# Kernel tuning notes

Hardware: AMD Instinct MI355X
Metric: run time of the kernel (lower is better)

Reference implementation:

```python
import jax, jax.numpy as jnp
import numpy as np

N_USERS = 100000
N_ITEMS = 50000
DIM = 64
HID = 64
E = 3200000
B = 16384


def setup_inputs() -> dict:
    key = jax.random.key(0)
    ks = jax.random.split(key, 16)
    N = N_USERS + N_ITEMS
    return {
        "users": jax.random.randint(ks[0], (B,), 0, N_USERS),
        "items": jax.random.randint(ks[1], (B,), 0, N_ITEMS),
        "edge_index": jax.random.randint(ks[2], (2, E), 0, N),
        "edge_weight": jax.random.uniform(ks[3], (E,), dtype=jnp.float32),
        # learned parameters
        "U": jax.random.normal(ks[4], (N_USERS, DIM), jnp.float32) * 0.1,
        "I": jax.random.normal(ks[5], (N_ITEMS, DIM), jnp.float32) * 0.1,
        "W0": jax.random.normal(ks[6], (DIM, HID), jnp.float32) / np.sqrt(DIM),
        "b0": jnp.zeros((HID,), jnp.float32),
        "g0": jnp.ones((HID,), jnp.float32),
        "be0": jnp.zeros((HID,), jnp.float32),
        "W1": jax.random.normal(ks[7], (HID, HID), jnp.float32) / np.sqrt(HID),
        "b1": jnp.zeros((HID,), jnp.float32),
        "g1": jnp.ones((HID,), jnp.float32),
        "be1": jnp.zeros((HID,), jnp.float32),
        "Wp": jax.random.normal(ks[8], (HID, DIM), jnp.float32) / np.sqrt(HID),
        "bp": jnp.zeros((DIM,), jnp.float32),
        "bu": jnp.zeros((N_USERS,), jnp.float32),
        "bi": jnp.zeros((N_ITEMS,), jnp.float32),
        "mu": jnp.zeros((), jnp.float32),
    }


def _layernorm(h, g, b, eps=1e-5):
    m = jnp.mean(h, axis=-1, keepdims=True)
    v = jnp.mean(jnp.square(h - m), axis=-1, keepdims=True)
    return (h - m) * jax.lax.rsqrt(v + eps) * g + b


def reference(users, items, edge_index, edge_weight, U, I,
              W0, b0, g0, be0, W1, b1, g1, be1, Wp, bp, bu, bi, mu):
    N = U.shape[0] + I.shape[0]
    x = jnp.concatenate([U, I], axis=0)  # [N, DIM]

    # GCN normalization with added self-loops (torch_geometric gcn_norm)
    loop = jnp.arange(N)
    src = jnp.concatenate([edge_index[0], loop])
    dst = jnp.concatenate([edge_index[1], loop])
    ew = jnp.concatenate([edge_weight, jnp.ones((N,), edge_weight.dtype)])
    deg = jax.ops.segment_sum(ew, dst, num_segments=N)
    dinv = jnp.where(deg > 0, jax.lax.rsqrt(deg), 0.0)
    norm = dinv[src] * ew * dinv[dst]  # [E+N]

    def conv(h, W, b):
        hw = h @ W  # [N, HID]
        msgs = norm[:, None] * hw[src]  # gather: [E+N, HID]
        return jax.ops.segment_sum(msgs, dst, num_segments=N) + b

    # layer 0: conv -> layernorm -> relu -> (dropout=identity, eval) -> residual
    h = x
    h_in = h
    h = conv(h, W0, b0)
    h = jax.nn.relu(_layernorm(h, g0, be0)) + h_in
    # layer 1
    h_in = h
    h = conv(h, W1, b1)
    h = jax.nn.relu(_layernorm(h, g1, be1)) + h_in

    h = h @ Wp + bp  # proj_out: [N, DIM]
    h_user = h[:U.shape[0]]
    h_item = h[U.shape[0]:]

    s = jnp.sum(h_user[users] * h_item[items], axis=-1)
    s = s + bu[users] + bi[items] + mu
    return jnp.clip(s, 1.0, 5.0)
```

## Files before the change

### kernel.cpp

```cpp
#include <hip/hip_runtime.h>

#define NU 100000
#define NI 50000
#define NN 150000
#define D  64
#define CAP 47
#define OVF_MAX 4096

#define BINSHIFT 9
#define BINW 512
#define NBINS 293
#define BINCAP 11448
#define STAGE_CAP 20
#define EPT 4
#define SPILL_CAP 262144

typedef unsigned int uint;
typedef unsigned short ushort;

__device__ __forceinline__ float wave_reduce_add(float v) {
    #pragma unroll
    for (int m = 32; m >= 1; m >>= 1) v += __shfl_xor(v, m, 64);
    return v;
}
__device__ __forceinline__ float bf2f(ushort u) {
    union { uint i; float f; } c; c.i = ((uint)u) << 16; return c.f;
}
__device__ __forceinline__ ushort f2bf(float f) {
    union { float f; uint i; } c; c.f = f;
    uint r = c.i + 0x7FFF + ((c.i >> 16) & 1);
    return (ushort)(r >> 16);
}
__device__ __forceinline__ float lane_bcast(float v, int l) {
    return __int_as_float(__builtin_amdgcn_readlane(__float_as_int(v), l));
}
__device__ __forceinline__ uint q14(float w) {
    int q = (int)(w * 16384.0f);
    q = (q < 0) ? 0 : (q > 16383 ? 16383 : q);
    return (uint)q;
}
__device__ __forceinline__ void spill_one(int d, uint s, float w,
        uint2* __restrict__ spill, int* __restrict__ spillcnt) {
    int si = atomicAdd(spillcnt, 1);
    if (si < SPILL_CAP) spill[si] = make_uint2(s | (q14(w) << 18), (uint)d);
}

__global__ __launch_bounds__(256) void k_bin(
        const int* __restrict__ src, const int* __restrict__ dst,
        const float* __restrict__ ew, int* __restrict__ bincur,
        uint2* __restrict__ binbuf, uint2* __restrict__ spill,
        int* __restrict__ spillcnt, int E) {
    __shared__ uint2 stage[NBINS][STAGE_CAP];
    __shared__ int scnt[NBINS];
    int t = threadIdx.x;
    for (int i = t; i < NBINS; i += 256) scnt[i] = 0;
    __syncthreads();
    const int batch = 256 * EPT;
    for (int base = blockIdx.x * batch; base < E; base += gridDim.x * batch) {
        int dd[EPT]; uint ss[EPT]; float ww[EPT]; int ok[EPT];
        #pragma unroll
        for (int k = 0; k < EPT; ++k) {
            int e = base + k * 256 + t;
            ok[k] = (e < E);
            if (ok[k]) { dd[k] = dst[e]; ss[k] = (uint)src[e]; ww[k] = ew[e]; }
        }
        #pragma unroll
        for (int k = 0; k < EPT; ++k) {
            if (!ok[k]) continue;
            int bin = dd[k] >> BINSHIFT;
            int slot = atomicAdd(&scnt[bin], 1);
            if (slot < STAGE_CAP) {
                stage[bin][slot] = make_uint2(
                    ss[k] | ((uint)(dd[k] & (BINW - 1)) << 18),
                    (uint)__float_as_int(ww[k]));
            } else {
                spill_one(dd[k], ss[k], ww[k], spill, spillcnt);
            }
        }
        __syncthreads();
        for (int bin = t; bin < NBINS; bin += 256) {
            int c = scnt[bin]; if (c > STAGE_CAP) c = STAGE_CAP;
            while (c >= 8) {
                int b0 = atomicAdd(&bincur[bin], 8);
                if (b0 + 8 <= BINCAP) {
                    uint4* o4 = (uint4*)(binbuf + (size_t)bin * BINCAP + b0);
                    uint2* s2 = &stage[bin][c - 8];
                    o4[0] = make_uint4(s2[0].x, s2[0].y, s2[1].x, s2[1].y);
                    o4[1] = make_uint4(s2[2].x, s2[2].y, s2[3].x, s2[3].y);
                    o4[2] = make_uint4(s2[4].x, s2[4].y, s2[5].x, s2[5].y);
                    o4[3] = make_uint4(s2[6].x, s2[6].y, s2[7].x, s2[7].y);
                } else {
                    for (int j = 0; j < 8; ++j) {
                        uint2 r = stage[bin][c - 8 + j];
                        spill_one((bin << BINSHIFT) + (int)(r.x >> 18),
                                  r.x & 0x3FFFFu, __int_as_float((int)r.y),
                                  spill, spillcnt);
                    }
                }
                c -= 8;
            }
            scnt[bin] = c;
        }
        __syncthreads();
    }
    for (int bin = t; bin < NBINS; bin += 256) {
        int c = scnt[bin]; if (c > STAGE_CAP) c = STAGE_CAP;
        if (c > 0) {
            int b0 = atomicAdd(&bincur[bin], c);
            for (int j = 0; j < c; ++j) {
                uint2 r = stage[bin][j];
                if (b0 + j < BINCAP) binbuf[(size_t)bin * BINCAP + b0 + j] = r;
                else spill_one((bin << BINSHIFT) + (int)(r.x >> 18),
                               r.x & 0x3FFFFu, __int_as_float((int)r.y),
                               spill, spillcnt);
            }
        }
    }
}

__global__ __launch_bounds__(256) void k_regroup(
        const int* __restrict__ bincur, const uint2* __restrict__ binbuf,
        uint* __restrict__ recs, int* __restrict__ cursor,
        int4* __restrict__ ovf, int* __restrict__ ovfcnt) {
    __shared__ uint image[256 * CAP];
    __shared__ int cnt[256];
    int t = threadIdx.x;
    int bin  = blockIdx.x >> 1;
    int half = blockIdx.x & 1;
    cnt[t] = 0;
    __syncthreads();
    int nrec = bincur[bin]; if (nrec > BINCAP) nrec = BINCAP;
    const uint2* bb = binbuf + (size_t)bin * BINCAP;
    for (int i = t; i < nrec; i += 256) {
        uint2 r = bb[i];
        int dlocal = (int)(r.x >> 18);
        if ((dlocal >> 8) == half) {
            int dl = dlocal & 255;
            int slot = atomicAdd(&cnt[dl], 1);
            uint s = r.x & 0x3FFFFu;
            float w = __int_as_float((int)r.y);
            if (slot < CAP) {
                image[dl * CAP + slot] = (q14(w) << 18) | s;
            } else {
                int d = (bin << BINSHIFT) + dlocal;
                int o = atomicAdd(ovfcnt, 1);
                if (o < OVF_MAX) ovf[o] = make_int4(d, (int)s, __float_as_int(w), 0);
            }
        }
    }
    __syncthreads();
    int dbase = (bin << BINSHIFT) + half * 256;
    int ndl = NN - dbase; if (ndl > 256) ndl = 256;
    if (ndl <= 0) return;
    if (t < ndl) cursor[dbase + t] = cnt[t];
    int tot = ndl * CAP;
    uint* out = recs + (size_t)dbase * CAP;
    for (int i = t; i < tot; i += 256) out[i] = image[i];
}

__global__ void k_spill_fix(const uint2* __restrict__ spill, const int* __restrict__ spillcnt,
                            uint* __restrict__ recs, int* __restrict__ cursor,
                            int4* __restrict__ ovf, int* __restrict__ ovfcnt) {
    int n = spillcnt[0]; if (n > SPILL_CAP) n = SPILL_CAP;
    for (int i = blockIdx.x * blockDim.x + threadIdx.x; i < n;
         i += gridDim.x * blockDim.x) {
        uint2 e = spill[i];
        int d = (int)e.y;
        uint s = e.x & 0x3FFFFu;
        uint q = e.x >> 18;
        int slot = atomicAdd(&cursor[d], 1);
        if (slot < CAP) recs[(size_t)d * CAP + slot] = (q << 18) | s;
        else {
            float w = (float)q * (1.0f / 16384.0f);
            int o = atomicAdd(ovfcnt, 1);
            if (o < OVF_MAX) ovf[o] = make_int4(d, (int)s, __float_as_int(w), 0);
        }
    }
}

__global__ void k_degdinv(const int* __restrict__ cursor, const uint* __restrict__ recs,
                          float* __restrict__ deg, float* __restrict__ dinv) {
    int lane = threadIdx.x & 63;
    int n = blockIdx.x * (blockDim.x >> 6) + (threadIdx.x >> 6);
    if (n >= NN) return;
    int cnt = cursor[n]; if (cnt > CAP) cnt = CAP;
    float w = 0.0f;
    if (lane < cnt) w = (float)(recs[(size_t)n * CAP + lane] >> 18) * (1.0f / 16384.0f);
    float s = wave_reduce_add(w);
    if (lane == 0) {
        deg[n] = s;
        dinv[n] = rsqrtf(s + 1.0f);
    }
}

__global__ void k_ovf_fix(const int4* __restrict__ ovf, const int* __restrict__ ovfcnt,
                          float* __restrict__ deg, float* __restrict__ dinv) {
    if (threadIdx.x != 0 || blockIdx.x != 0) return;
    int n = ovfcnt[0]; if (n > OVF_MAX) n = OVF_MAX;
    for (int i = 0; i < n; ++i) {
        int d = ovf[i].x;
        float dg = deg[d] + __int_as_float(ovf[i].z);
        deg[d] = dg;
        dinv[d] = rsqrtf(dg + 1.0f);
    }
}

__global__ void k_gemm(const float* __restrict__ h, const float* __restrict__ U,
                       const float* __restrict__ I, const float* __restrict__ W,
                       const float* __restrict__ dinv, ushort* __restrict__ out) {
    __shared__ float Ws[64 * 64];
    for (int i = threadIdx.x; i < 64 * 64; i += blockDim.x) Ws[i] = W[i];
    __syncthreads();
    int lane = threadIdx.x & 63;
    int wpb = blockDim.x >> 6;
    int wid = blockIdx.x * wpb + (threadIdx.x >> 6);
    int tw = gridDim.x * wpb;
    for (int n = wid; n < NN; n += tw) {
        float xv;
        if (h) xv = h[(size_t)n * D + lane];
        else   xv = (n < NU) ? U[(size_t)n * D + lane] : I[(size_t)(n - NU) * D + lane];
        float acc = 0.f;
        #pragma unroll
        for (int k = 0; k < 64; ++k)
            acc = fmaf(lane_bcast(xv, k), Ws[k * 64 + lane], acc);
        out[(size_t)n * D + lane] = f2bf(acc * dinv[n]);
    }
}

__device__ __forceinline__ float conv_accum(int n, int lane,
        const ushort* __restrict__ hw2b, const int* __restrict__ cursor,
        const uint* __restrict__ recs, const int4* __restrict__ ovf,
        const int* __restrict__ ovfcnt) {
    int cnt = __builtin_amdgcn_readfirstlane(cursor[n]);
    if (cnt > CAP) cnt = CAP;
    uint rv = (lane < cnt) ? recs[(size_t)n * CAP + lane] : 0u;
    float a = bf2f(hw2b[(size_t)n * D + lane]);
    int cp = (cnt + 7) & ~7;
    for (int j0 = 0; j0 < cp; j0 += 8) {
        #pragma unroll
        for (int k = 0; k < 8; ++k) {
            uint r = (uint)__builtin_amdgcn_readlane((int)rv, j0 + k);
            int   s = (int)(r & 0x3FFFFu);
            float w = (float)(r >> 18) * (1.0f / 16384.0f);
            a = fmaf(w, bf2f(hw2b[(size_t)s * D + lane]), a);
        }
    }
    int novf = __builtin_amdgcn_readfirstlane(ovfcnt[0]);
    if (novf > 0) {
        if (novf > OVF_MAX) novf = OVF_MAX;
        for (int j = 0; j < novf; ++j) {
            int4 e = ovf[j];
            if (e.x == n) a = fmaf(__int_as_float(e.z),
                                   bf2f(hw2b[(size_t)e.y * D + lane]), a);
        }
    }
    return a;
}

__device__ __forceinline__ float ln_relu(float v, int lane,
        const float* __restrict__ g, const float* __restrict__ be) {
    float m = wave_reduce_add(v) * (1.0f / 64.0f);
    float dv = v - m;
    float var = wave_reduce_add(dv * dv) * (1.0f / 64.0f);
    return fmaxf(dv * rsqrtf(var + 1e-5f) * g[lane] + be[lane], 0.0f);
}

__global__ __launch_bounds__(256) void k_conv1(
        const ushort* __restrict__ hw2b, const int* __restrict__ cursor,
        const uint* __restrict__ recs, const int4* __restrict__ ovf,
        const int* __restrict__ ovfcnt, const float* __restrict__ dinv,
        const float* __restrict__ b, const float* __restrict__ g,
        const float* __restrict__ be, const float* __restrict__ U,
        const float* __restrict__ I, float* __restrict__ out) {
    int lane = threadIdx.x & 63;
    int n = __builtin_amdgcn_readfirstlane(blockIdx.x * 4 + (threadIdx.x >> 6));
    if (n >= NN) return;
    float a = conv_accum(n, lane, hw2b, cursor, recs, ovf, ovfcnt);
    float v = a * dinv[n] + b[lane];
    float y = ln_relu(v, lane, g, be);
    float r = (n < NU) ? U[(size_t)n * D + lane] : I[(size_t)(n - NU) * D + lane];
    out[(size_t)n * D + lane] = y + r;
}

__global__ __launch_bounds__(256) void k_conv2s(
        const ushort* __restrict__ hw2b, const int* __restrict__ cursor,
        const uint* __restrict__ recs, const int4* __restrict__ ovf,
        const int* __restrict__ ovfcnt, const float* __restrict__ dinv,
        const float* __restrict__ b, const float* __restrict__ g,
        const float* __restrict__ be, const int* __restrict__ users,
        const int* __restrict__ items, const float* __restrict__ h1,
        float* __restrict__ h2s, int B) {
    int lane = threadIdx.x & 63;
    int p = blockIdx.x * 4 + (threadIdx.x >> 6);
    if (p >= 2 * B) return;
    int n = (p < B) ? users[p] : NU + items[p - B];
    n = __builtin_amdgcn_readfirstlane(n);
    float a = conv_accum(n, lane, hw2b, cursor, recs, ovf, ovfcnt);
    float v = a * dinv[n] + b[lane];
    float y = ln_relu(v, lane, g, be);
    h2s[(size_t)p * D + lane] = y + h1[(size_t)n * D + lane];
}

__global__ void k_score(const float* __restrict__ h2s, const int* __restrict__ users,
                        const int* __restrict__ items, const float* __restrict__ Wp,
                        const float* __restrict__ bp, const float* __restrict__ bu,
                        const float* __restrict__ bi, const float* __restrict__ mu,
                        float* __restrict__ out, int B) {
    __shared__ float Ws[64 * 64];
    for (int i = threadIdx.x; i < 64 * 64; i += blockDim.x) Ws[i] = Wp[i];
    __syncthreads();
    int lane = threadIdx.x & 63;
    int wpb = blockDim.x >> 6;
    int wid = blockIdx.x * wpb + (threadIdx.x >> 6);
    int tw = gridDim.x * wpb;
    for (int p = wid; p < B; p += tw) {
        float hu = h2s[(size_t)p * D + lane];
        float hi = h2s[(size_t)(B + p) * D + lane];
        float pu = bp[lane], pi = bp[lane];
        #pragma unroll
        for (int k = 0; k < 64; ++k) {
            float wv = Ws[k * 64 + lane];
            pu = fmaf(lane_bcast(hu, k), wv, pu);
            pi = fmaf(lane_bcast(hi, k), wv, pi);
        }
        float s = wave_reduce_add(pu * pi);
        if (lane == 0) {
            s += bu[users[p]] + bi[items[p]] + mu[0];
            out[p] = fminf(fmaxf(s, 1.0f), 5.0f);
        }
    }
}

extern "C" void kernel_launch(void* const* d_in, const int* in_sizes, int n_in,
                              void* d_out, int out_size, void* d_ws, size_t ws_size,
                              hipStream_t stream) {
    const int*   users = (const int*)d_in[0];
    const int*   items = (const int*)d_in[1];
    const int*   ei2   = (const int*)d_in[2];
    const float* ew    = (const float*)d_in[3];
    const float* U     = (const float*)d_in[4];
    const float* I     = (const float*)d_in[5];
    const float* W0    = (const float*)d_in[6];
    const float* b0    = (const float*)d_in[7];
    const float* g0    = (const float*)d_in[8];
    const float* be0   = (const float*)d_in[9];
    const float* W1    = (const float*)d_in[10];
    const float* b1    = (const float*)d_in[11];
    const float* g1    = (const float*)d_in[12];
    const float* be1   = (const float*)d_in[13];
    const float* Wp    = (const float*)d_in[14];
    const float* bp    = (const float*)d_in[15];
    const float* bu    = (const float*)d_in[16];
    const float* bi    = (const float*)d_in[17];
    const float* mu    = (const float*)d_in[18];

    int B = in_sizes[0];
    int E = in_sizes[2] / 2;
    const int* srcp = ei2;
    const int* dstp = ei2 + E;

    char* p = (char*)d_ws;
    auto alloc = [&](size_t bytes) -> char* {
        char* r = p;
        p += (bytes + 255) & ~(size_t)255;
        return r;
    };
    float*  deg     = (float*)alloc((size_t)NN * 4);
    int*    cursor  = (int*)  alloc((size_t)NN * 4);
    float*  dinv    = (float*)alloc((size_t)NN * 4);
    int*    ovfcnt  = (int*)  alloc(256);
    int*    spillcnt= (int*)  alloc(256);
    int*    bincur  = (int*)  alloc((size_t)NBINS * 4);
    int4*   ovf     = (int4*) alloc((size_t)OVF_MAX * 16);
    uint2*  spill   = (uint2*)alloc((size_t)SPILL_CAP * 8);
    uint2*  binbuf  = (uint2*)alloc((size_t)NBINS * BINCAP * 8);
    uint*   recs    = (uint*) alloc((size_t)NN * CAP * 4);
    ushort* hw2b    = (ushort*)alloc((size_t)NN * D * 2);
    float*  h1      = (float*)alloc((size_t)NN * D * 4);
    float*  h2s     = (float*)alloc((size_t)2 * B * D * 4);

    hipMemsetAsync(bincur, 0, (size_t)NBINS * 4, stream);
    hipMemsetAsync(spillcnt, 0, 4, stream);
    hipMemsetAsync(ovfcnt, 0, 4, stream);

    int gW = (NN + 3) / 4;
    int gS = (2 * B + 3) / 4;

    k_bin<<<256, 256, 0, stream>>>(srcp, dstp, ew, bincur, binbuf,
                                   spill, spillcnt, E);
    k_regroup<<<NBINS * 2, 256, 0, stream>>>(bincur, binbuf, recs, cursor,
                                             ovf, ovfcnt);
    k_spill_fix<<<32, 256, 0, stream>>>(spill, spillcnt, recs, cursor,
                                        ovf, ovfcnt);
    k_degdinv<<<gW, 256, 0, stream>>>(cursor, recs, deg, dinv);
    k_ovf_fix<<<1, 64, 0, stream>>>(ovf, ovfcnt, deg, dinv);

    k_gemm<<<2048, 256, 0, stream>>>(nullptr, U, I, W0, dinv, hw2b);
    k_conv1<<<gW, 256, 0, stream>>>(hw2b, cursor, recs, ovf, ovfcnt, dinv,
                                    b0, g0, be0, U, I, h1);
    k_gemm<<<2048, 256, 0, stream>>>(h1, U, I, W1, dinv, hw2b);
    k_conv2s<<<gS, 256, 0, stream>>>(hw2b, cursor, recs, ovf, ovfcnt, dinv,
                                     b1, g1, be1, users, items, h1, h2s, B);

    k_score<<<512, 256, 0, stream>>>(h2s, users, items, Wp, bp, bu, bi, mu,
                                     (float*)d_out, B);
}
```

Measured before the change: 476.1 us.

## Fold spill fix and degree computation into regroup; half-wave packed bf16 gather

The spill-fix, degree and overflow-fix kernels are merged into k_regroup. Each block now also scans the global spill list for its own destination range and computes dinv from its shared-memory image, adding overflow weights through a shared accumulator. The conv gather splits each wave into two 32-lane halves that handle alternate edges, loading packed bf16 pairs and combining the halves with a shuffle. k_bin gets more blocks and the three counter memsets become one. In exchange, every regroup block scans the whole spill list, which is redundant work when the spill is large.

```diff
diff --git a/kernel.cpp b/kernel.cpp
--- a/kernel.cpp
+++ b/kernel.cpp
@@ -18,13 +18,10 @@
 typedef unsigned int uint;
 typedef unsigned short ushort;
 
-__device__ __forceinline__ float wave_reduce_add(float v) {
+__device__ __forceinline__ float half_reduce_add(float v) {
     #pragma unroll
-    for (int m = 32; m >= 1; m >>= 1) v += __shfl_xor(v, m, 64);
+    for (int m = 16; m >= 1; m >>= 1) v += __shfl_xor(v, m, 64);
     return v;
-}
-__device__ __forceinline__ float bf2f(ushort u) {
-    union { uint i; float f; } c; c.i = ((uint)u) << 16; return c.f;
 }
 __device__ __forceinline__ ushort f2bf(float f) {
     union { float f; uint i; } c; c.f = f;
@@ -120,89 +117,70 @@
 
 __global__ __launch_bounds__(256) void k_regroup(
         const int* __restrict__ bincur, const uint2* __restrict__ binbuf,
+        const uint2* __restrict__ spill, const int* __restrict__ spillcnt,
         uint* __restrict__ recs, int* __restrict__ cursor,
-        int4* __restrict__ ovf, int* __restrict__ ovfcnt) {
+        float* __restrict__ dinv, int4* __restrict__ ovf,
+        int* __restrict__ ovfcnt) {
     __shared__ uint image[256 * CAP];
     __shared__ int cnt[256];
+    __shared__ float ovfw[256];
     int t = threadIdx.x;
     int bin  = blockIdx.x >> 1;
     int half = blockIdx.x & 1;
-    cnt[t] = 0;
+    cnt[t] = 0; ovfw[t] = 0.0f;
     __syncthreads();
+    int dbase = (bin << BINSHIFT) + half * 256;
     int nrec = bincur[bin]; if (nrec > BINCAP) nrec = BINCAP;
     const uint2* bb = binbuf + (size_t)bin * BINCAP;
     for (int i = t; i < nrec; i += 256) {
         uint2 r = bb[i];
         int dlocal = (int)(r.x >> 18);
-        if ((dlocal >> 8) == half) {
-            int dl = dlocal & 255;
-            int slot = atomicAdd(&cnt[dl], 1);
-            uint s = r.x & 0x3FFFFu;
-            float w = __int_as_float((int)r.y);
-            if (slot < CAP) {
-                image[dl * CAP + slot] = (q14(w) << 18) | s;
-            } else {
-                int d = (bin << BINSHIFT) + dlocal;
-                int o = atomicAdd(ovfcnt, 1);
-                if (o < OVF_MAX) ovf[o] = make_int4(d, (int)s, __float_as_int(w), 0);
-            }
+        if ((dlocal >> 8) != half) continue;
+        int dl = dlocal & 255;
+        int slot = atomicAdd(&cnt[dl], 1);
+        uint s = r.x & 0x3FFFFu;
+        float w = __int_as_float((int)r.y);
+        if (slot < CAP) image[dl * CAP + slot] = (q14(w) << 18) | s;
+        else {
+            atomicAdd(&ovfw[dl], w);
+            int o = atomicAdd(ovfcnt, 1);
+            if (o < OVF_MAX)
+                ovf[o] = make_int4((bin << BINSHIFT) + dlocal, (int)s,
+                                   __float_as_int(w), 0);
+        }
+    }
+    int ns = spillcnt[0]; if (ns > SPILL_CAP) ns = SPILL_CAP;
+    for (int i = t; i < ns; i += 256) {
+        uint2 e = spill[i];
+        int d = (int)e.y;
+        if (d < dbase || d >= dbase + 256) continue;
+        int dl = d - dbase;
+        int slot = atomicAdd(&cnt[dl], 1);
+        uint s = e.x & 0x3FFFFu;
+        uint q = e.x >> 18;
+        if (slot < CAP) image[dl * CAP + slot] = (q << 18) | s;
+        else {
+            float w = (float)q * (1.0f / 16384.0f);
+            atomicAdd(&ovfw[dl], w);
+            int o = atomicAdd(ovfcnt, 1);
+            if (o < OVF_MAX) ovf[o] = make_int4(d, (int)s, __float_as_int(w), 0);
         }
     }
     __syncthreads();
-    int dbase = (bin << BINSHIFT) + half * 256;
     int ndl = NN - dbase; if (ndl > 256) ndl = 256;
     if (ndl <= 0) return;
-    if (t < ndl) cursor[dbase + t] = cnt[t];
+    if (t < ndl) {
+        int c = cnt[t];
+        cursor[dbase + t] = c;
+        if (c > CAP) c = CAP;
+        uint sq = 0;
+        for (int j = 0; j < c; ++j) sq += image[t * CAP + j] >> 18;
+        float dg = (float)sq * (1.0f / 16384.0f) + ovfw[t];
+        dinv[dbase + t] = rsqrtf(dg + 1.0f);
+    }
     int tot = ndl * CAP;
     uint* out = recs + (size_t)dbase * CAP;
     for (int i = t; i < tot; i += 256) out[i] = image[i];
-}
-
-__global__ void k_spill_fix(const uint2* __restrict__ spill, const int* __restrict__ spillcnt,
-                            uint* __restrict__ recs, int* __restrict__ cursor,
-                            int4* __restrict__ ovf, int* __restrict__ ovfcnt) {
-    int n = spillcnt[0]; if (n > SPILL_CAP) n = SPILL_CAP;
-    for (int i = blockIdx.x * blockDim.x + threadIdx.x; i < n;
-         i += gridDim.x * blockDim.x) {
-        uint2 e = spill[i];
-        int d = (int)e.y;
-        uint s = e.x & 0x3FFFFu;
-        uint q = e.x >> 18;
-        int slot = atomicAdd(&cursor[d], 1);
-        if (slot < CAP) recs[(size_t)d * CAP + slot] = (q << 18) | s;
-        else {
-            float w = (float)q * (1.0f / 16384.0f);
-            int o = atomicAdd(ovfcnt, 1);
-            if (o < OVF_MAX) ovf[o] = make_int4(d, (int)s, __float_as_int(w), 0);
-        }
-    }
-}
-
-__global__ void k_degdinv(const int* __restrict__ cursor, const uint* __restrict__ recs,
-                          float* __restrict__ deg, float* __restrict__ dinv) {
-    int lane = threadIdx.x & 63;
-    int n = blockIdx.x * (blockDim.x >> 6) + (threadIdx.x >> 6);
-    if (n >= NN) return;
-    int cnt = cursor[n]; if (cnt > CAP) cnt = CAP;
-    float w = 0.0f;
-    if (lane < cnt) w = (float)(recs[(size_t)n * CAP + lane] >> 18) * (1.0f / 16384.0f);
-    float s = wave_reduce_add(w);
-    if (lane == 0) {
-        deg[n] = s;
-        dinv[n] = rsqrtf(s + 1.0f);
-    }
-}
-
-__global__ void k_ovf_fix(const int4* __restrict__ ovf, const int* __restrict__ ovfcnt,
-                          float* __restrict__ deg, float* __restrict__ dinv) {
-    if (threadIdx.x != 0 || blockIdx.x != 0) return;
-    int n = ovfcnt[0]; if (n > OVF_MAX) n = OVF_MAX;
-    for (int i = 0; i < n; ++i) {
-        int d = ovf[i].x;
-        float dg = deg[d] + __int_as_float(ovf[i].z);
-        deg[d] = dg;
-        dinv[d] = rsqrtf(dg + 1.0f);
-    }
 }
 
 __global__ void k_gemm(const float* __restrict__ h, const float* __restrict__ U,
@@ -218,7 +196,8 @@
     for (int n = wid; n < NN; n += tw) {
         float xv;
         if (h) xv = h[(size_t)n * D + lane];
-        else   xv = (n < NU) ? U[(size_t)n * D + lane] : I[(size_t)(n - NU) * D + lane];
+        else   xv = (n < NU) ? U[(size_t)n * D + lane]
+                             : I[(size_t)(n - NU) * D + lane];
         float acc = 0.f;
         #pragma unroll
         for (int k = 0; k < 64; ++k)
@@ -227,46 +206,65 @@
     }
 }
 
-__device__ __forceinline__ float conv_accum(int n, int lane,
-        const ushort* __restrict__ hw2b, const int* __restrict__ cursor,
+__device__ __forceinline__ float2 conv_accum2(int n, int lane,
+        const uint* __restrict__ hw2p, const int* __restrict__ cursor,
         const uint* __restrict__ recs, const int4* __restrict__ ovf,
         const int* __restrict__ ovfcnt) {
     int cnt = __builtin_amdgcn_readfirstlane(cursor[n]);
     if (cnt > CAP) cnt = CAP;
     uint rv = (lane < cnt) ? recs[(size_t)n * CAP + lane] : 0u;
-    float a = bf2f(hw2b[(size_t)n * D + lane]);
-    int cp = (cnt + 7) & ~7;
-    for (int j0 = 0; j0 < cp; j0 += 8) {
-        #pragma unroll
-        for (int k = 0; k < 8; ++k) {
-            uint r = (uint)__builtin_amdgcn_readlane((int)rv, j0 + k);
-            int   s = (int)(r & 0x3FFFFu);
-            float w = (float)(r >> 18) * (1.0f / 16384.0f);
-            a = fmaf(w, bf2f(hw2b[(size_t)s * D + lane]), a);
-        }
-    }
+    int laneoff = lane & 31;
+    int ap = ((lane >> 5) & 1) << 2;
+    float ax = 0.f, ay = 0.f;
+    int cp = (cnt + 1) & ~1;
+    for (int j = 0; j < cp; j += 2) {
+        uint r = (uint)__builtin_amdgcn_ds_bpermute(ap, (int)rv);
+        ap += 8;
+        int   s = (int)(r & 0x3FFFFu);
+        float w = (float)(r >> 18) * (1.0f / 16384.0f);
+        uint x = hw2p[(size_t)s * 32 + laneoff];
+        ax = fmaf(w, __int_as_float((int)(x << 16)), ax);
+        ay = fmaf(w, __int_as_float((int)(x & 0xFFFF0000u)), ay);
+    }
+    ax += __shfl_xor(ax, 32, 64);
+    ay += __shfl_xor(ay, 32, 64);
+    uint xs = hw2p[(size_t)n * 32 + laneoff];
+    ax += __int_as_float((int)(xs << 16));
+    ay += __int_as_float((int)(xs & 0xFFFF0000u));
     int novf = __builtin_amdgcn_readfirstlane(ovfcnt[0]);
     if (novf > 0) {
         if (novf > OVF_MAX) novf = OVF_MAX;
         for (int j = 0; j < novf; ++j) {
             int4 e = ovf[j];
-            if (e.x == n) a = fmaf(__int_as_float(e.z),
-                                   bf2f(hw2b[(size_t)e.y * D + lane]), a);
-        }
-    }
-    return a;
-}
-
-__device__ __forceinline__ float ln_relu(float v, int lane,
-        const float* __restrict__ g, const float* __restrict__ be) {
-    float m = wave_reduce_add(v) * (1.0f / 64.0f);
-    float dv = v - m;
-    float var = wave_reduce_add(dv * dv) * (1.0f / 64.0f);
-    return fmaxf(dv * rsqrtf(var + 1e-5f) * g[lane] + be[lane], 0.0f);
+            if (e.x == n) {
+                float w = __int_as_float(e.z);
+                uint x = hw2p[(size_t)e.y * 32 + laneoff];
+                ax = fmaf(w, __int_as_float((int)(x << 16)), ax);
+                ay = fmaf(w, __int_as_float((int)(x & 0xFFFF0000u)), ay);
+            }
+        }
+    }
+    return make_float2(ax, ay);
+}
+
+__device__ __forceinline__ float2 ln_relu2(float2 a, float di, int p,
+        const float* __restrict__ b, const float* __restrict__ g,
+        const float* __restrict__ be) {
+    float2 bb = ((const float2*)b)[p];
+    float v0 = fmaf(a.x, di, bb.x);
+    float v1 = fmaf(a.y, di, bb.y);
+    float m = half_reduce_add(v0 + v1) * (1.0f / 64.0f);
+    float d0 = v0 - m, d1 = v1 - m;
+    float var = half_reduce_add(d0 * d0 + d1 * d1) * (1.0f / 64.0f);
+    float rs = rsqrtf(var + 1e-5f);
+    float2 gg = ((const float2*)g)[p];
+    float2 ee = ((const float2*)be)[p];
+    return make_float2(fmaxf(fmaf(d0 * rs, gg.x, ee.x), 0.0f),
+                       fmaxf(fmaf(d1 * rs, gg.y, ee.y), 0.0f));
 }
 
 __global__ __launch_bounds__(256) void k_conv1(
-        const ushort* __restrict__ hw2b, const int* __restrict__ cursor,
+        const uint* __restrict__ hw2p, const int* __restrict__ cursor,
         const uint* __restrict__ recs, const int4* __restrict__ ovf,
         const int* __restrict__ ovfcnt, const float* __restrict__ dinv,
         const float* __restrict__ b, const float* __restrict__ g,
@@ -275,15 +273,17 @@
     int lane = threadIdx.x & 63;
     int n = __builtin_amdgcn_readfirstlane(blockIdx.x * 4 + (threadIdx.x >> 6));
     if (n >= NN) return;
-    float a = conv_accum(n, lane, hw2b, cursor, recs, ovf, ovfcnt);
-    float v = a * dinv[n] + b[lane];
-    float y = ln_relu(v, lane, g, be);
-    float r = (n < NU) ? U[(size_t)n * D + lane] : I[(size_t)(n - NU) * D + lane];
-    out[(size_t)n * D + lane] = y + r;
+    float2 a = conv_accum2(n, lane, hw2p, cursor, recs, ovf, ovfcnt);
+    int p = lane & 31;
+    float2 y = ln_relu2(a, dinv[n], p, b, g, be);
+    const float* R = (n < NU) ? (U + (size_t)n * D) : (I + (size_t)(n - NU) * D);
+    float2 rr = ((const float2*)R)[p];
+    if (lane < 32)
+        ((float2*)out)[(size_t)n * 32 + p] = make_float2(y.x + rr.x, y.y + rr.y);
 }
 
 __global__ __launch_bounds__(256) void k_conv2s(
-        const ushort* __restrict__ hw2b, const int* __restrict__ cursor,
+        const uint* __restrict__ hw2p, const int* __restrict__ cursor,
         const uint* __restrict__ recs, const int4* __restrict__ ovf,
         const int* __restrict__ ovfcnt, const float* __restrict__ dinv,
         const float* __restrict__ b, const float* __restrict__ g,
@@ -295,10 +295,12 @@
     if (p >= 2 * B) return;
     int n = (p < B) ? users[p] : NU + items[p - B];
     n = __builtin_amdgcn_readfirstlane(n);
-    float a = conv_accum(n, lane, hw2b, cursor, recs, ovf, ovfcnt);
-    float v = a * dinv[n] + b[lane];
-    float y = ln_relu(v, lane, g, be);
-    h2s[(size_t)p * D + lane] = y + h1[(size_t)n * D + lane];
+    float2 a = conv_accum2(n, lane, hw2p, cursor, recs, ovf, ovfcnt);
+    int q = lane & 31;
+    float2 y = ln_relu2(a, dinv[n], q, b, g, be);
+    float2 rr = ((const float2*)h1)[(size_t)n * 32 + q];
+    if (lane < 32)
+        ((float2*)h2s)[(size_t)p * 32 + q] = make_float2(y.x + rr.x, y.y + rr.y);
 }
 
 __global__ void k_score(const float* __restrict__ h2s, const int* __restrict__ users,
@@ -323,10 +325,12 @@
             pu = fmaf(lane_bcast(hu, k), wv, pu);
             pi = fmaf(lane_bcast(hi, k), wv, pi);
         }
-        float s = wave_reduce_add(pu * pi);
+        float t = pu * pi;
+        #pragma unroll
+        for (int m = 32; m >= 1; m >>= 1) t += __shfl_xor(t, m, 64);
         if (lane == 0) {
-            s += bu[users[p]] + bi[items[p]] + mu[0];
-            out[p] = fminf(fmaxf(s, 1.0f), 5.0f);
+            t += bu[users[p]] + bi[items[p]] + mu[0];
+            out[p] = fminf(fmaxf(t, 1.0f), 5.0f);
         }
     }
 }
@@ -365,12 +369,12 @@
         p += (bytes + 255) & ~(size_t)255;
         return r;
     };
-    float*  deg     = (float*)alloc((size_t)NN * 4);
+    int*    cbuf    = (int*)  alloc((size_t)(NBINS + 8) * 4);
+    int*    bincur  = cbuf;
+    int*    spillcnt= cbuf + NBINS;
+    int*    ovfcnt  = cbuf + NBINS + 1;
     int*    cursor  = (int*)  alloc((size_t)NN * 4);
     float*  dinv    = (float*)alloc((size_t)NN * 4);
-    int*    ovfcnt  = (int*)  alloc(256);
-    int*    spillcnt= (int*)  alloc(256);
-    int*    bincur  = (int*)  alloc((size_t)NBINS * 4);
     int4*   ovf     = (int4*) alloc((size_t)OVF_MAX * 16);
     uint2*  spill   = (uint2*)alloc((size_t)SPILL_CAP * 8);
     uint2*  binbuf  = (uint2*)alloc((size_t)NBINS * BINCAP * 8);
@@ -378,28 +382,23 @@
     ushort* hw2b    = (ushort*)alloc((size_t)NN * D * 2);
     float*  h1      = (float*)alloc((size_t)NN * D * 4);
     float*  h2s     = (float*)alloc((size_t)2 * B * D * 4);
-
-    hipMemsetAsync(bincur, 0, (size_t)NBINS * 4, stream);
-    hipMemsetAsync(spillcnt, 0, 4, stream);
-    hipMemsetAsync(ovfcnt, 0, 4, stream);
+    const uint* hw2p = (const uint*)hw2b;
+
+    hipMemsetAsync(cbuf, 0, (size_t)(NBINS + 8) * 4, stream);
 
     int gW = (NN + 3) / 4;
     int gS = (2 * B + 3) / 4;
 
-    k_bin<<<256, 256, 0, stream>>>(srcp, dstp, ew, bincur, binbuf,
+    k_bin<<<768, 256, 0, stream>>>(srcp, dstp, ew, bincur, binbuf,
                                    spill, spillcnt, E);
-    k_regroup<<<NBINS * 2, 256, 0, stream>>>(bincur, binbuf, recs, cursor,
-                                             ovf, ovfcnt);
-    k_spill_fix<<<32, 256, 0, stream>>>(spill, spillcnt, recs, cursor,
-                                        ovf, ovfcnt);
-    k_degdinv<<<gW, 256, 0, stream>>>(cursor, recs, deg, dinv);
-    k_ovf_fix<<<1, 64, 0, stream>>>(ovf, ovfcnt, deg, dinv);
+    k_regroup<<<NBINS * 2, 256, 0, stream>>>(bincur, binbuf, spill, spillcnt,
+                                             recs, cursor, dinv, ovf, ovfcnt);
 
     k_gemm<<<2048, 256, 0, stream>>>(nullptr, U, I, W0, dinv, hw2b);
-    k_conv1<<<gW, 256, 0, stream>>>(hw2b, cursor, recs, ovf, ovfcnt, dinv,
+    k_conv1<<<gW, 256, 0, stream>>>(hw2p, cursor, recs, ovf, ovfcnt, dinv,
                                     b0, g0, be0, U, I, h1);
     k_gemm<<<2048, 256, 0, stream>>>(h1, U, I, W1, dinv, hw2b);
-    k_conv2s<<<gS, 256, 0, stream>>>(hw2b, cursor, recs, ovf, ovfcnt, dinv,
+    k_conv2s<<<gS, 256, 0, stream>>>(hw2p, cursor, recs, ovf, ovfcnt, dinv,
                                      b1, g1, be1, users, items, h1, h2s, B);
 
     k_score<<<512, 256, 0, stream>>>(h2s, users, items, Wp, bp, bu, bi, mu,
```

New measurement: 507.1 us. 6.5% more time.
